# Kernel optimization log

Measured on AMD Instinct MI355X. Metric: run time of the kernel, lower is better.

The kernel has to match this reference:

```python
import jax, jax.numpy as jnp
import numpy as np

B, N, K = 4, 4096, 16
C_IN, C_OUT = 128, 128
H1, H2 = 256, 256
IN_SZ = 2 * C_IN  # key_feats='self' -> concat(self feats, neighbor feats)


def setup_inputs() -> dict:
    key = jax.random.key(0)
    ks = jax.random.split(key, 12)
    s = 1.0 / np.sqrt(IN_SZ)
    inp = {
        "keys": jax.random.normal(ks[0], (B, N, 3), jnp.float32),
        "points": jax.random.normal(ks[1], (B, N, 3), jnp.float32),
        "feats": jax.random.normal(ks[2], (B, N, C_IN), jnp.float32),
        "n_idxs": jax.random.randint(ks[3], (B, N, K), 0, N, jnp.int32),
        "neighbor_valid": jax.random.randint(ks[4], (B, N, K), 0, 2, jnp.int32),
        "W1": jax.random.uniform(ks[5], (IN_SZ, H1), jnp.float32, -s, s),
        "b1": jnp.zeros((H1,), jnp.float32),
        "W2": jax.random.uniform(ks[6], (H1, H2), jnp.float32, -1/np.sqrt(H1), 1/np.sqrt(H1)),
        "b2": jnp.zeros((H2,), jnp.float32),
        "W3": jax.random.uniform(ks[7], (H2, C_OUT), jnp.float32, -1/np.sqrt(H2), 1/np.sqrt(H2)),
        "b3": jnp.zeros((C_OUT,), jnp.float32),
    }
    return inp


def reference(keys, points, feats, n_idxs, neighbor_valid, W1, b1, W2, b2, W3, b3):
    # gather neighbor features: feats[bb, n_idxs] -> [B, N, K, C_IN]
    bb = jnp.arange(feats.shape[0])[:, None, None]
    neighbor_feats = feats[bb, n_idxs]
    # key_feats='self': broadcast query's own feats over neighbor dim, concat
    exp_feats = jnp.broadcast_to(feats[:, :, None, :], neighbor_feats.shape)
    pairs = jnp.concatenate([exp_feats, neighbor_feats], axis=-1)  # [B,N,K,2C]
    # SetTransform MLP per edge (reduction='none')
    h = jax.nn.relu(jnp.einsum("bnki,ih->bnkh", pairs, W1) + b1)
    h = jax.nn.relu(jnp.einsum("bnkh,hj->bnkj", h, W2) + b2)
    edges = jnp.einsum("bnkj,jo->bnko", h, W3) + b3  # [B,N,K,C_OUT]
    # mask invalid neighbors and reduce over neighbor dim
    mask = neighbor_valid[..., None].astype(edges.dtype)
    reduced = jnp.sum(edges * mask, axis=2)  # [B,N,C_OUT]
    return reduced
```

## Files before the change

### kernel.cpp

```cpp
#include <hip/hip_runtime.h>
#include <stdint.h>

#define Cc 128

typedef __attribute__((ext_vector_type(4))) float f32x4;
typedef __attribute__((ext_vector_type(16))) float f32x16;
typedef __attribute__((ext_vector_type(8))) short s16x8;

__device__ __forceinline__ unsigned int asu(float f) { union { float f; unsigned int u; } v; v.f = f; return v.u; }
__device__ __forceinline__ float asf(unsigned int u) { union { unsigned int u; float f; } v; v.u = u; return v.f; }

__device__ __forceinline__ unsigned short f2bf_rne(float f) {
  unsigned int u = asu(f);
  unsigned int r = u + 0x7FFFu + ((u >> 16) & 1u);
  return (unsigned short)(r >> 16);
}

__device__ __forceinline__ unsigned int pk2(float lo, float hi) {
  return __builtin_amdgcn_perm(asu(hi) + 0x8000u, asu(lo) + 0x8000u, 0x07060302u);
}

__device__ __forceinline__ unsigned int cvt1(unsigned int a, unsigned int b) {
  float alo = asf(a << 16), ahi = asf(a & 0xFFFF0000u);
  float blo = asf(b << 16), bhi = asf(b & 0xFFFF0000u);
  float lo = fmaxf(alo + blo, 0.f);
  float hi = fmaxf(ahi + bhi, 0.f);
  return pk2(lo, hi);
}

#define MFMA16(a, b, c) __builtin_amdgcn_mfma_f32_16x16x32_bf16((a), (b), (c), 0, 0, 0)
#define MFMA32(a, b, c) __builtin_amdgcn_mfma_f32_32x32x16_bf16((a), (b), (c), 0, 0, 0)

__global__ void pack_kernel(const float* __restrict__ W1,
                            const float* __restrict__ W2,
                            const float* __restrict__ W3,
                            const float* __restrict__ b2,
                            const float* __restrict__ b3,
                            unsigned short* __restrict__ W1p,
                            unsigned short* __restrict__ W2p,
                            unsigned short* __restrict__ W3p,
                            float* __restrict__ t3v,
                            float* __restrict__ u3v) {
  int blk = blockIdx.x, t = threadIdx.x;
  if (blk < 32) {
    int f = blk * 256 + t;
    int l = f & 63, ct = (f >> 6) & 31, kt = f >> 11;
    int col = ct * 16 + (l & 15);
    int k0 = kt * 32 + ((l >> 4) << 3);
    unsigned short tmp[8];
#pragma unroll
    for (int j = 0; j < 8; ++j) {
      int k = k0 + j;
      float v = (col < 256) ? W1[k * 256 + col] : W1[(128 + k) * 256 + (col - 256)];
      tmp[j] = f2bf_rne(v);
    }
    *(uint4*)(W1p + f * 8) = *(uint4*)tmp;
  } else if (blk < 64) {
    int f = (blk - 32) * 256 + t;
    int l = f & 63, ct = (f >> 6) & 7, kt = f >> 9;
    int col = ct * 32 + (l & 31);
    int k0 = kt * 16 + ((l >> 5) << 3);
    unsigned short tmp[8];
#pragma unroll
    for (int j = 0; j < 8; ++j) tmp[j] = f2bf_rne(W2[(k0 + j) * 256 + col]);
    *(uint4*)(W2p + f * 8) = *(uint4*)tmp;
  } else if (blk < 80) {
    int f = (blk - 64) * 256 + t;
    int l = f & 63, ct = (f >> 6) & 7, kt = f >> 9;
    int col = ct * 16 + (l & 15);
    int k0 = kt * 32 + ((l >> 4) << 3);
    unsigned short tmp[8];
#pragma unroll
    for (int j = 0; j < 8; ++j) tmp[j] = f2bf_rne(W3[(k0 + j) * 128 + col]);
    *(uint4*)(W3p + f * 8) = *(uint4*)tmp;
  } else {
    __shared__ float part[256];
    if (t < 256) {
      int col = t & 127, half = t >> 7;
      float s = 0.f;
      for (int j = half * 128; j < half * 128 + 128; ++j)
        s += fmaxf(b2[j], 0.f) * W3[j * 128 + col];
      part[t] = s;
    }
    __syncthreads();
    if (t < 128) {
      float c3 = part[t] + part[t + 128];
      t3v[t] = b3[t] + c3;
      u3v[t] = 16.f * c3;
    }
  }
}

__global__ __launch_bounds__(256, 4) void k1_gemm(
    const float* __restrict__ feats,
    const unsigned short* __restrict__ W1p,
    const float* __restrict__ b1,
    unsigned short* __restrict__ A_ws,
    unsigned short* __restrict__ B_ws) {
  __shared__ __attribute__((aligned(16))) unsigned short cs[32 * 512];
  char* cb = (char*)cs;
  int m0 = blockIdx.x * 32;
  int t = threadIdx.x, w = t >> 6, l = t & 63, lr = l & 15, lg = l >> 4;
  f32x4 zero4 = {0.f, 0.f, 0.f, 0.f};
  f32x4 acc[2][8];
#pragma unroll
  for (int i = 0; i < 2; ++i)
#pragma unroll
    for (int j = 0; j < 8; ++j) acc[i][j] = zero4;

  for (int kt = 0; kt < 4; ++kt) {
    s16x8 a[2];
#pragma unroll
    for (int rt = 0; rt < 2; ++rt) {
      const float* fr = feats + (m0 + rt * 16 + lr) * 128 + kt * 32 + lg * 8;
      float4 f0 = *(const float4*)fr;
      float4 f1 = *(const float4*)(fr + 4);
      uint4 pk;
      pk.x = pk2(f0.x, f0.y);
      pk.y = pk2(f0.z, f0.w);
      pk.z = pk2(f1.x, f1.y);
      pk.w = pk2(f1.z, f1.w);
      *(uint4*)&a[rt] = pk;
    }
#pragma unroll
    for (int ctl = 0; ctl < 8; ++ctl) {
      s16x8 bf = *(const s16x8*)(W1p + (((kt * 32) + (w * 8 + ctl)) * 64 + l) * 8);
#pragma unroll
      for (int rt = 0; rt < 2; ++rt)
        acc[rt][ctl] = MFMA16(a[rt], bf, acc[rt][ctl]);
    }
  }

#pragma unroll
  for (int ctl = 0; ctl < 8; ++ctl) {
    int col = w * 128 + ctl * 16 + lr;
    float bias = (col < 256) ? b1[col] : 0.f;
#pragma unroll
    for (int rt = 0; rt < 2; ++rt) {
#pragma unroll
      for (int reg = 0; reg < 4; ++reg) {
        int node = rt * 16 + lg * 4 + reg;
        float v = acc[rt][ctl][reg] + bias;
        unsigned short bv = (unsigned short)((asu(v) + 0x8000u) >> 16);
        *(unsigned short*)(cb + ((node * 1024 + col * 2) ^ ((node & 7) << 4))) = bv;
      }
    }
  }
  __syncthreads();
#pragma unroll
  for (int i = 0; i < 8; ++i) {
    int row = i * 4 + w;
    uint4 v = *(const uint4*)(cb + row * 1024 + ((l * 16) ^ ((row & 7) << 4)));
    int node = m0 + row;
    unsigned short* dst = (l < 32) ? (A_ws + node * 256 + l * 8)
                                   : (B_ws + node * 256 + (l - 32) * 8);
    *(uint4*)dst = v;
  }
}

__global__ __launch_bounds__(512, 6) void k2_fused(
    const unsigned short* __restrict__ A_ws,
    const unsigned short* __restrict__ B_ws,
    const unsigned short* __restrict__ W2p,
    const unsigned short* __restrict__ W3p,
    const int* __restrict__ n_idxs,
    const int* __restrict__ valid,
    const float* __restrict__ b2,
    const float* __restrict__ t3v,
    const float* __restrict__ u3v,
    float* __restrict__ out) {
  __shared__ __attribute__((aligned(16))) unsigned short h1s[64 * 128];
  __shared__ __attribute__((aligned(16))) unsigned short gs[16 * 264];
  __shared__ float nvf[4];
  char* h1b = (char*)h1s;
  char* gb = (char*)gs;

  int t = threadIdx.x, w = t >> 6, l = t & 63;
  int bid = blockIdx.x;
  int wg = (bid & 7) * 512 + (bid >> 3);
  int qbase = wg * 4, ebase = wg * 64;
  int bN = qbase & ~4095;

  if (t < 384) {
    int row = 4 + (t >> 5), ch = t & 31;
    *(f32x4*)(gb + row * 528 + ch * 16) = f32x4{0.f, 0.f, 0.f, 0.f};
  }
  if (t < 4) {
    int s = 0;
#pragma unroll
    for (int k = 0; k < 16; ++k) s += valid[ebase + t * 16 + k];
    nvf[t] = (float)s;
  }

  int r = t >> 3, c8 = t & 7;
  int nb = n_idxs[ebase + r];
  int vld = valid[ebase + r];
  const unsigned short* pa = A_ws + (qbase + (r >> 4)) * 256;
  const unsigned short* pb = B_ws + (bN + nb) * 256;
  int swz = (r & 15) << 4;

  int hi = l >> 5, col = l & 31;
  int row0 = col, row1 = 32 + col;
  int base0 = row0 * 256, sz0 = (row0 & 15) << 4;
  int base1 = row1 * 256, sz1 = (row1 & 15) << 4;

  f32x16 acc0 = {0.f,0.f,0.f,0.f,0.f,0.f,0.f,0.f,0.f,0.f,0.f,0.f,0.f,0.f,0.f,0.f};
  f32x16 acc1 = acc0;

#pragma unroll
  for (int p = 0; p < 2; ++p) {
#pragma unroll
    for (int i = 0; i < 2; ++i) {
      int ch = c8 + i * 8;
      uint4 av = *(const uint4*)(pa + p * 128 + ch * 8);
      uint4 bv = *(const uint4*)(pb + p * 128 + ch * 8);
      uint4 o;
      o.x = cvt1(av.x, bv.x);
      o.y = cvt1(av.y, bv.y);
      o.z = cvt1(av.z, bv.z);
      o.w = cvt1(av.w, bv.w);
      if (!vld) { o.x = 0u; o.y = 0u; o.z = 0u; o.w = 0u; }
      *(uint4*)(h1b + ((r * 256 + ch * 16) ^ swz)) = o;
    }
    __syncthreads();
#pragma unroll
    for (int kt = 0; kt < 8; ++kt) {
      int kb = kt * 32 + hi * 16;
      s16x8 a0 = *(const s16x8*)(h1b + (base0 + (kb ^ sz0)));
      s16x8 a1 = *(const s16x8*)(h1b + (base1 + (kb ^ sz1)));
      s16x8 bf = *(const s16x8*)(W2p + (((p * 8 + kt) * 8 + w) * 64 + l) * 8);
      acc0 = MFMA32(a0, bf, acc0);
      acc1 = MFMA32(a1, bf, acc1);
    }
    __syncthreads();
  }

  {
    float bias = b2[w * 32 + col];
    float s0 = 0.f, s1 = 0.f, s2 = 0.f, s3 = 0.f;
#pragma unroll
    for (int g = 0; g < 8; ++g) {
      s0 += fmaxf(acc0[g] + bias, 0.f);
      s1 += fmaxf(acc0[8 + g] + bias, 0.f);
      s2 += fmaxf(acc1[g] + bias, 0.f);
      s3 += fmaxf(acc1[8 + g] + bias, 0.f);
    }
    s0 += __shfl_xor(s0, 32);
    s1 += __shfl_xor(s1, 32);
    s2 += __shfl_xor(s2, 32);
    s3 += __shfl_xor(s3, 32);
    if (l < 32) {
      int cb2 = (w * 32 + col) * 2;
      *(unsigned short*)(gb + 0 * 528 + cb2) = f2bf_rne(s0);
      *(unsigned short*)(gb + 1 * 528 + cb2) = f2bf_rne(s1);
      *(unsigned short*)(gb + 2 * 528 + cb2) = f2bf_rne(s2);
      *(unsigned short*)(gb + 3 * 528 + cb2) = f2bf_rne(s3);
    }
  }
  __syncthreads();

  {
    int lr = l & 15, lg = l >> 4;
    f32x4 acc3 = {0.f, 0.f, 0.f, 0.f};
#pragma unroll
    for (int kt = 0; kt < 8; ++kt) {
      s16x8 a = *(const s16x8*)(gb + lr * 528 + kt * 64 + lg * 16);
      s16x8 bf = *(const s16x8*)(W3p + ((kt * 8 + w) * 64 + l) * 8);
      acc3 = MFMA16(a, bf, acc3);
    }
    if (lg == 0) {
      int col3 = w * 16 + lr;
      float tt = t3v[col3], uu = u3v[col3];
#pragma unroll
      for (int reg = 0; reg < 4; ++reg)
        out[(qbase + reg) * Cc + col3] = acc3[reg] + nvf[reg] * tt - uu;
    }
  }
}

extern "C" void kernel_launch(void* const* d_in, const int* in_sizes, int n_in,
                              void* d_out, int out_size, void* d_ws, size_t ws_size,
                              hipStream_t stream) {
  const float* feats = (const float*)d_in[2];
  const int* n_idxs = (const int*)d_in[3];
  const int* valid = (const int*)d_in[4];
  const float* W1 = (const float*)d_in[5];
  const float* b1 = (const float*)d_in[6];
  const float* W2 = (const float*)d_in[7];
  const float* b2 = (const float*)d_in[8];
  const float* W3 = (const float*)d_in[9];
  const float* b3 = (const float*)d_in[10];
  float* out = (float*)d_out;

  char* ws = (char*)d_ws;
  unsigned short* A_ws = (unsigned short*)(ws);
  unsigned short* B_ws = (unsigned short*)(ws + (8u << 20));
  unsigned short* W1p  = (unsigned short*)(ws + (16u << 20));
  unsigned short* W2p  = (unsigned short*)(ws + (16u << 20) + (128u << 10));
  unsigned short* W3p  = (unsigned short*)(ws + (16u << 20) + (256u << 10));
  float* t3v = (float*)(ws + (16u << 20) + (320u << 10));
  float* u3v = (float*)(ws + (16u << 20) + (321u << 10));

  pack_kernel<<<81, 256, 0, stream>>>(W1, W2, W3, b2, b3, W1p, W2p, W3p, t3v, u3v);
  k1_gemm<<<512, 256, 0, stream>>>(feats, W1p, b1, A_ws, B_ws);
  k2_fused<<<4096, 512, 0, stream>>>(A_ws, B_ws, W2p, W3p, n_idxs, valid, b2, t3v, u3v, out);
}
```

Before: 186.9 us.

## Process eight query nodes per block with full-K staged tile in k2

The fused second kernel now handles 8 queries (128 edges) per workgroup instead of 4, staging the whole 256-wide hidden tile in LDS at once rather than in two halves. Each wave computes a 64x64 output tile (2x2 MFMAs) so every W2 fragment load is reused across twice as many rows, and one barrier pair is removed. The cost is 64KB of LDS per block and more accumulator registers, so fewer blocks fit per CU (launch bounds lowered from 6 to 4) and the grid is halved.

```diff
diff --git a/kernel.cpp b/kernel.cpp
--- a/kernel.cpp
+++ b/kernel.cpp
@@ -158,7 +158,7 @@
   }
 }
 
-__global__ __launch_bounds__(512, 6) void k2_fused(
+__global__ __launch_bounds__(512, 4) void k2_fused(
     const unsigned short* __restrict__ A_ws,
     const unsigned short* __restrict__ B_ws,
     const unsigned short* __restrict__ W2p,
@@ -169,92 +169,108 @@
     const float* __restrict__ t3v,
     const float* __restrict__ u3v,
     float* __restrict__ out) {
-  __shared__ __attribute__((aligned(16))) unsigned short h1s[64 * 128];
+  __shared__ __attribute__((aligned(16))) unsigned short h1s[128 * 256];
   __shared__ __attribute__((aligned(16))) unsigned short gs[16 * 264];
-  __shared__ float nvf[4];
+  __shared__ float nvf[8];
   char* h1b = (char*)h1s;
   char* gb = (char*)gs;
 
   int t = threadIdx.x, w = t >> 6, l = t & 63;
   int bid = blockIdx.x;
-  int wg = (bid & 7) * 512 + (bid >> 3);
-  int qbase = wg * 4, ebase = wg * 64;
+  int wg = (bid & 7) * 256 + (bid >> 3);
+  int qbase = wg * 8, ebase = wg * 128;
   int bN = qbase & ~4095;
 
-  if (t < 384) {
-    int row = 4 + (t >> 5), ch = t & 31;
+  if (t < 256) {
+    int row = 8 + (t >> 5), ch = t & 31;
     *(f32x4*)(gb + row * 528 + ch * 16) = f32x4{0.f, 0.f, 0.f, 0.f};
   }
-  if (t < 4) {
+  if (t < 8) {
     int s = 0;
 #pragma unroll
     for (int k = 0; k < 16; ++k) s += valid[ebase + t * 16 + k];
     nvf[t] = (float)s;
   }
 
-  int r = t >> 3, c8 = t & 7;
-  int nb = n_idxs[ebase + r];
-  int vld = valid[ebase + r];
-  const unsigned short* pa = A_ws + (qbase + (r >> 4)) * 256;
-  const unsigned short* pb = B_ws + (bN + nb) * 256;
-  int swz = (r & 15) << 4;
-
-  int hi = l >> 5, col = l & 31;
-  int row0 = col, row1 = 32 + col;
-  int base0 = row0 * 256, sz0 = (row0 & 15) << 4;
-  int base1 = row1 * 256, sz1 = (row1 & 15) << 4;
-
-  f32x16 acc0 = {0.f,0.f,0.f,0.f,0.f,0.f,0.f,0.f,0.f,0.f,0.f,0.f,0.f,0.f,0.f,0.f};
-  f32x16 acc1 = acc0;
-
-#pragma unroll
-  for (int p = 0; p < 2; ++p) {
-#pragma unroll
-    for (int i = 0; i < 2; ++i) {
-      int ch = c8 + i * 8;
-      uint4 av = *(const uint4*)(pa + p * 128 + ch * 8);
-      uint4 bv = *(const uint4*)(pb + p * 128 + ch * 8);
+  {
+    int r = t >> 2, sub = t & 3;
+    int nb = n_idxs[ebase + r];
+    int vld = valid[ebase + r];
+    const unsigned short* pa = A_ws + (qbase + (r >> 4)) * 256 + sub * 64;
+    const unsigned short* pb = B_ws + (bN + nb) * 256 + sub * 64;
+    int rbase = r * 512, swz = (r & 15) << 4;
+#pragma unroll
+    for (int i = 0; i < 8; ++i) {
+      uint4 av = *(const uint4*)(pa + i * 8);
+      uint4 bv = *(const uint4*)(pb + i * 8);
       uint4 o;
       o.x = cvt1(av.x, bv.x);
       o.y = cvt1(av.y, bv.y);
       o.z = cvt1(av.z, bv.z);
       o.w = cvt1(av.w, bv.w);
       if (!vld) { o.x = 0u; o.y = 0u; o.z = 0u; o.w = 0u; }
-      *(uint4*)(h1b + ((r * 256 + ch * 16) ^ swz)) = o;
-    }
-    __syncthreads();
-#pragma unroll
-    for (int kt = 0; kt < 8; ++kt) {
-      int kb = kt * 32 + hi * 16;
-      s16x8 a0 = *(const s16x8*)(h1b + (base0 + (kb ^ sz0)));
-      s16x8 a1 = *(const s16x8*)(h1b + (base1 + (kb ^ sz1)));
-      s16x8 bf = *(const s16x8*)(W2p + (((p * 8 + kt) * 8 + w) * 64 + l) * 8);
-      acc0 = MFMA32(a0, bf, acc0);
-      acc1 = MFMA32(a1, bf, acc1);
-    }
-    __syncthreads();
+      *(uint4*)(h1b + rbase + ((sub * 128 + i * 16) ^ swz)) = o;
+    }
+  }
+  __syncthreads();
+
+  int cg = w & 3, rh = w >> 2;
+  int col = l & 31, hi = l >> 5;
+  int row0 = rh * 64 + col, row1 = row0 + 32;
+  int base0 = row0 * 512, sz0 = (row0 & 15) << 4;
+  int base1 = row1 * 512, sz1 = (row1 & 15) << 4;
+
+  f32x16 acc00 = {0.f,0.f,0.f,0.f,0.f,0.f,0.f,0.f,0.f,0.f,0.f,0.f,0.f,0.f,0.f,0.f};
+  f32x16 acc01 = acc00, acc10 = acc00, acc11 = acc00;
+
+#pragma unroll
+  for (int kt = 0; kt < 16; ++kt) {
+    int kb = kt * 32 + hi * 16;
+    s16x8 a0 = *(const s16x8*)(h1b + base0 + (kb ^ sz0));
+    s16x8 a1 = *(const s16x8*)(h1b + base1 + (kb ^ sz1));
+    s16x8 b0 = *(const s16x8*)(W2p + ((kt * 8 + cg * 2 + 0) * 64 + l) * 8);
+    s16x8 b1 = *(const s16x8*)(W2p + ((kt * 8 + cg * 2 + 1) * 64 + l) * 8);
+    acc00 = MFMA32(a0, b0, acc00);
+    acc01 = MFMA32(a0, b1, acc01);
+    acc10 = MFMA32(a1, b0, acc10);
+    acc11 = MFMA32(a1, b1, acc11);
   }
 
   {
-    float bias = b2[w * 32 + col];
+    float bias0 = b2[cg * 64 + col];
+    float bias1 = b2[cg * 64 + 32 + col];
     float s0 = 0.f, s1 = 0.f, s2 = 0.f, s3 = 0.f;
+    float s4 = 0.f, s5 = 0.f, s6 = 0.f, s7 = 0.f;
 #pragma unroll
     for (int g = 0; g < 8; ++g) {
-      s0 += fmaxf(acc0[g] + bias, 0.f);
-      s1 += fmaxf(acc0[8 + g] + bias, 0.f);
-      s2 += fmaxf(acc1[g] + bias, 0.f);
-      s3 += fmaxf(acc1[8 + g] + bias, 0.f);
+      s0 += fmaxf(acc00[g] + bias0, 0.f);
+      s1 += fmaxf(acc00[8 + g] + bias0, 0.f);
+      s2 += fmaxf(acc10[g] + bias0, 0.f);
+      s3 += fmaxf(acc10[8 + g] + bias0, 0.f);
+      s4 += fmaxf(acc01[g] + bias1, 0.f);
+      s5 += fmaxf(acc01[8 + g] + bias1, 0.f);
+      s6 += fmaxf(acc11[g] + bias1, 0.f);
+      s7 += fmaxf(acc11[8 + g] + bias1, 0.f);
     }
     s0 += __shfl_xor(s0, 32);
     s1 += __shfl_xor(s1, 32);
     s2 += __shfl_xor(s2, 32);
     s3 += __shfl_xor(s3, 32);
+    s4 += __shfl_xor(s4, 32);
+    s5 += __shfl_xor(s5, 32);
+    s6 += __shfl_xor(s6, 32);
+    s7 += __shfl_xor(s7, 32);
     if (l < 32) {
-      int cb2 = (w * 32 + col) * 2;
-      *(unsigned short*)(gb + 0 * 528 + cb2) = f2bf_rne(s0);
-      *(unsigned short*)(gb + 1 * 528 + cb2) = f2bf_rne(s1);
-      *(unsigned short*)(gb + 2 * 528 + cb2) = f2bf_rne(s2);
-      *(unsigned short*)(gb + 3 * 528 + cb2) = f2bf_rne(s3);
+      int q0 = rh * 4;
+      int c0 = (cg * 64 + col) * 2, c1 = (cg * 64 + 32 + col) * 2;
+      *(unsigned short*)(gb + (q0 + 0) * 528 + c0) = f2bf_rne(s0);
+      *(unsigned short*)(gb + (q0 + 1) * 528 + c0) = f2bf_rne(s1);
+      *(unsigned short*)(gb + (q0 + 2) * 528 + c0) = f2bf_rne(s2);
+      *(unsigned short*)(gb + (q0 + 3) * 528 + c0) = f2bf_rne(s3);
+      *(unsigned short*)(gb + (q0 + 0) * 528 + c1) = f2bf_rne(s4);
+      *(unsigned short*)(gb + (q0 + 1) * 528 + c1) = f2bf_rne(s5);
+      *(unsigned short*)(gb + (q0 + 2) * 528 + c1) = f2bf_rne(s6);
+      *(unsigned short*)(gb + (q0 + 3) * 528 + c1) = f2bf_rne(s7);
     }
   }
   __syncthreads();
@@ -268,12 +284,14 @@
       s16x8 bf = *(const s16x8*)(W3p + ((kt * 8 + w) * 64 + l) * 8);
       acc3 = MFMA16(a, bf, acc3);
     }
-    if (lg == 0) {
+    if (lg < 2) {
       int col3 = w * 16 + lr;
       float tt = t3v[col3], uu = u3v[col3];
 #pragma unroll
-      for (int reg = 0; reg < 4; ++reg)
-        out[(qbase + reg) * Cc + col3] = acc3[reg] + nvf[reg] * tt - uu;
+      for (int reg = 0; reg < 4; ++reg) {
+        int q = lg * 4 + reg;
+        out[(qbase + q) * Cc + col3] = acc3[reg] + nvf[q] * tt - uu;
+      }
     }
   }
 }
@@ -303,5 +321,5 @@
 
   pack_kernel<<<81, 256, 0, stream>>>(W1, W2, W3, b2, b3, W1p, W2p, W3p, t3v, u3v);
   k1_gemm<<<512, 256, 0, stream>>>(feats, W1p, b1, A_ws, B_ws);
-  k2_fused<<<4096, 512, 0, stream>>>(A_ws, B_ws, W2p, W3p, n_idxs, valid, b2, t3v, u3v, out);
-}
+  k2_fused<<<2048, 512, 0, stream>>>(A_ws, B_ws, W2p, W3p, n_idxs, valid, b2, t3v, u3v, out);
+}
```

After: 190.8 us. +2.1%, slower.
